# Kernel optimization log

Measured on AMD Instinct MI355X. Metric: run time of the kernel, lower is better.

## Reference

```python
import jax, jax.numpy as jnp
import numpy as np

P, N, D = 8, 1024, 768
H = 12
HS = D // H
SCALE = float(HS ** 0.5)  # NOTE: original multiplies by sqrt(head_size)


def setup_inputs() -> dict:
    key = jax.random.key(0)
    k1, k2, k3 = jax.random.split(key, 3)
    pixel_values = jax.random.normal(k1, (P, N, D), dtype=jnp.float32)
    attention_mask = jnp.zeros((P, 1, 1, N), dtype=jnp.float32)
    qkv_w = jax.random.normal(k2, (D, 3 * D), dtype=jnp.float32) * 0.02
    qkv_b = jnp.zeros((3 * D,), dtype=jnp.float32)
    proj_w = jax.random.normal(k3, (D, D), dtype=jnp.float32) * 0.02
    proj_b = jnp.zeros((D,), dtype=jnp.float32)
    return {
        "pixel_values": pixel_values,
        "attention_mask": attention_mask,
        "qkv_w": qkv_w,
        "qkv_b": qkv_b,
        "proj_w": proj_w,
        "proj_b": proj_b,
    }


def reference(pixel_values, attention_mask, qkv_w, qkv_b, proj_w, proj_b):
    p, n, d = pixel_values.shape
    # fused QKV projection: (p, n, 3d) -> (3, p, H, n, hs)
    mixed = pixel_values @ qkv_w + qkv_b
    mixed = mixed.reshape(p, n, 3, H, HS).transpose(2, 0, 3, 1, 4)
    q, k, v = mixed[0], mixed[1], mixed[2]
    # scores: (p, H, n, n); original multiplies by sqrt(head_size)
    scores = jnp.einsum("phqd,phkd->phqk", q, k) * SCALE
    probs = jax.nn.softmax(scores, axis=-1)
    # dropout p=0 (identity in eval); mask added POST-softmax, per source
    probs = probs + attention_mask
    ctx = jnp.einsum("phqk,phkd->phqd", probs, v)
    ctx = ctx.transpose(0, 2, 1, 3).reshape(p, n, d)
    out = ctx @ proj_w + proj_b
    return out
```

## Files before the change

### kernel.cpp

```cpp
#include <hip/hip_runtime.h>
#include <hip/hip_bf16.h>
#include <cstdint>
#include <math.h>

constexpr int PB = 8;
constexpr int NS = 1024;
constexpr int DM = 768;
constexpr int NH = 12;
constexpr int HSZ = 64;
constexpr float QS    = 11.541560327111707f;
constexpr float EOFFL = 126.95716359822878f;

typedef short    bf16x8 __attribute__((ext_vector_type(8)));
typedef _Float16 half8  __attribute__((ext_vector_type(8)));
typedef __fp16   fp16x2 __attribute__((ext_vector_type(2)));
typedef float    floatx4 __attribute__((ext_vector_type(4)));

#if __has_builtin(__builtin_amdgcn_exp2f)
#define EXP2(x) __builtin_amdgcn_exp2f(x)
#else
#define EXP2(x) exp2f(x)
#endif

__device__ __forceinline__ ushort f2h(float x) {
    _Float16 h = (_Float16)x;
    return *reinterpret_cast<ushort*>(&h);
}
__device__ __forceinline__ float h2f(ushort u) {
    _Float16 h = __builtin_bit_cast(_Float16, u);
    return (float)h;
}
__device__ __forceinline__ ushort f2bf(float x) {
    __hip_bfloat16 b = __float2bfloat16(x);
    return *reinterpret_cast<ushort*>(&b);
}
__device__ __forceinline__ float bf2f(ushort u) {
    __hip_bfloat16 b = *reinterpret_cast<__hip_bfloat16*>(&u);
    return __bfloat162float(b);
}
__device__ __forceinline__ unsigned int pk2h(float a, float b) {
    fp16x2 h = __builtin_amdgcn_cvt_pkrtz(a, b);
    return __builtin_bit_cast(unsigned int, h);
}

#define GLDS(g, l)                                                             \
    __builtin_amdgcn_global_load_lds(                                          \
        (const __attribute__((address_space(1))) void*)(g),                    \
        (__attribute__((address_space(3))) void*)(l), 16, 0, 0)

__global__ void split_kernel(const float* __restrict__ x, ushort* __restrict__ hf,
                             int n4)
{
    int i = blockIdx.x * blockDim.x + threadIdx.x;
    const int stride = gridDim.x * blockDim.x;
    for (; i < n4; i += stride) {
        const float4 v = ((const float4*)x)[i];
        ((ushort4*)hf)[i] = ushort4{f2h(v.x), f2h(v.y), f2h(v.z), f2h(v.w)};
    }
}

__global__ void splitT_kernel(const float* __restrict__ w, ushort* __restrict__ fT,
                              int K, int N)
{
    __shared__ float tile[32][33];
    const int tx = threadIdx.x, ty = threadIdx.y;
    const int bx = blockIdx.x, by = blockIdx.y;
    #pragma unroll
    for (int r = 0; r < 4; ++r)
        tile[ty + r*8][tx] = w[(size_t)(by*32 + ty + r*8) * N + bx*32 + tx];
    __syncthreads();
    #pragma unroll
    for (int r = 0; r < 4; ++r) {
        const int n = bx*32 + ty + r*8;
        const int k = by*32 + tx;
        fT[(size_t)n * K + k] = f2h(tile[tx][ty + r*8]);
    }
}

template <int MODE>
__global__ __launch_bounds__(256, 3)
void gemm_f16(const ushort* __restrict__ Af, const ushort* __restrict__ Bf,
              const float* __restrict__ bias, float* __restrict__ outf,
              ushort* __restrict__ qf, ushort* __restrict__ kf,
              ushort* __restrict__ vt, int K)
{
    __shared__ __align__(16) ushort As[128*64];
    __shared__ __align__(16) ushort Bs[128*64];

    const int t    = threadIdx.x;
    const int w    = t >> 6;
    const int lane = t & 63;
    const int l15  = lane & 15;
    const int quad = lane >> 4;
    const int wm = w >> 1, wn = w & 1;
    const int m0 = blockIdx.x * 128, n0 = blockIdx.y * 128;

    floatx4 acc[4][4];
    #pragma unroll
    for (int i = 0; i < 4; ++i)
        #pragma unroll
        for (int j = 0; j < 4; ++j) acc[i][j] = floatx4{0.f, 0.f, 0.f, 0.f};

    const int srow8 = lane >> 3;
    const int sslot = lane & 7;

    for (int k0 = 0; k0 < K; k0 += 64) {
        #pragma unroll
        for (int j = 0; j < 4; ++j) {
            const int row = w*32 + j*8 + srow8;
            const int seg = sslot ^ (row & 7);
            const int ldst = (w*32 + j*8) * 64;
            GLDS(Af + (size_t)(m0 + row) * K + k0 + seg*8, As + ldst);
            GLDS(Bf + (size_t)(n0 + row) * K + k0 + seg*8, Bs + ldst);
        }
        __syncthreads();

        #pragma unroll
        for (int h2 = 0; h2 < 2; ++h2) {
            half8 fa[4], fb[4];
            #pragma unroll
            for (int i = 0; i < 4; ++i) {
                const int sl = ((h2*4 + quad) ^ (l15 & 7)) * 8;
                fa[i] = *(const half8*)(As + (wm*64 + i*16 + l15) * 64 + sl);
                fb[i] = *(const half8*)(Bs + (wn*64 + i*16 + l15) * 64 + sl);
            }
            #pragma unroll
            for (int mt = 0; mt < 4; ++mt)
                #pragma unroll
                for (int nt = 0; nt < 4; ++nt)
                    acc[mt][nt] = __builtin_amdgcn_mfma_f32_16x16x32_f16(fa[mt], fb[nt], acc[mt][nt], 0, 0, 0);
        }
        __syncthreads();
    }

    if (MODE == 0) {
        #pragma unroll
        for (int nt = 0; nt < 4; ++nt) {
            const int col = n0 + wn*64 + nt*16 + l15;
            const float bval = bias[col];
            #pragma unroll
            for (int mt = 0; mt < 4; ++mt) {
                const int row0 = m0 + wm*64 + mt*16 + quad*4;
                #pragma unroll
                for (int r = 0; r < 4; ++r)
                    outf[(size_t)(row0 + r) * DM + col] = acc[mt][nt][r] + bval;
            }
        }
    } else {
        const int jbase = n0 + wn*64;
        const int c  = jbase / DM;
        const int hh = (jbase % DM) >> 6;
        const int pp = (m0 + wm*64) >> 10;
        const size_t head = (size_t)pp * NH + hh;
        if (c < 2) {
            ushort* dst = (c == 0 ? qf : kf);
            const float qscale = (c == 0) ? QS : 1.0f;
            #pragma unroll
            for (int nt = 0; nt < 4; ++nt) {
                const int s = nt*16 + l15;
                const float bval = bias[jbase + s];
                #pragma unroll
                for (int mt = 0; mt < 4; ++mt) {
                    const int tok0 = m0 + wm*64 + mt*16 + quad*4;
                    const int nn0  = tok0 & 1023;
                    #pragma unroll
                    for (int r = 0; r < 4; ++r)
                        dst[(head*NS + nn0 + r) * HSZ + s] = f2h((acc[mt][nt][r] + bval) * qscale);
                }
            }
        } else {
            #pragma unroll
            for (int nt = 0; nt < 4; ++nt) {
                const int s = nt*16 + l15;
                const float bval = bias[jbase + s];
                #pragma unroll
                for (int mt = 0; mt < 4; ++mt) {
                    const int tok0 = m0 + wm*64 + mt*16 + quad*4;
                    const int nn0  = tok0 & 1023;
                    ushort4 pk;
                    pk.x = f2bf(acc[mt][nt][0] + bval);
                    pk.y = f2bf(acc[mt][nt][1] + bval);
                    pk.z = f2bf(acc[mt][nt][2] + bval);
                    pk.w = f2bf(acc[mt][nt][3] + bval);
                    *(ushort4*)(vt + (head*HSZ + s) * NS + nn0) = pk;
                }
            }
        }
    }
}

__global__ void mv_kernel(const float* __restrict__ mask, const ushort* __restrict__ vt,
                          float* __restrict__ mv)
{
    __shared__ float red[4][64];
    const int ph = blockIdx.x;
    const int t  = threadIdx.x;
    const int c  = t & 63, part = t >> 6;
    const ushort* vrow = vt + ((size_t)ph * HSZ + c) * NS + part * 256;
    const float*  mrow = mask + (size_t)(ph / NH) * NS + part * 256;
    float acc = 0.f;
    for (int k = 0; k < 256; k += 4) {
        const ushort4 v4 = *(const ushort4*)(vrow + k);
        const float4  m4 = *(const float4*)(mrow + k);
        acc += m4.x * bf2f(v4.x) + m4.y * bf2f(v4.y)
             + m4.z * bf2f(v4.z) + m4.w * bf2f(v4.w);
    }
    red[part][c] = acc;
    __syncthreads();
    if (t < 64)
        mv[(size_t)ph * HSZ + t] = red[0][t] + red[1][t] + red[2][t] + red[3][t];
}

__global__ __launch_bounds__(256, 5)
void attn_mfma_kernel(const ushort* __restrict__ qf, const ushort* __restrict__ kf,
                      const ushort* __restrict__ vt, const float* __restrict__ mv,
                      ushort* __restrict__ ctx)
{
    __shared__ __align__(16) ushort khs[64*64];
    __shared__ __align__(16) ushort vs [64*64];

    const int t    = threadIdx.x;
    const int w    = t >> 6;
    const int lane = t & 63;
    const int l15  = lane & 15;
    const int quad = lane >> 4;
    const int ph = blockIdx.x, qt = blockIdx.y;
    const int h  = ph % NH,    p  = ph / NH;
    const size_t headoff = ((size_t)p * NH + h) * (size_t)(NS * HSZ);

    const ushort* qb = qf + headoff + (size_t)(qt*64 + w*16 + l15) * HSZ + quad*8;
    const half8 qfr0 = *(const half8*)(qb);
    const half8 qfr1 = *(const half8*)(qb + 32);

    floatx4 o[4];
    float lsum = 0.f;
    #pragma unroll
    for (int tc = 0; tc < 4; ++tc) o[tc] = floatx4{0.f, 0.f, 0.f, 0.f};

    const int srow8 = lane >> 3;
    const int sslot = lane & 7;
    const int xs = l15 & 7;

    for (int kt = 0; kt < 16; ++kt) {
        __syncthreads();
        #pragma unroll
        for (int j = 0; j < 2; ++j) {
            const int row  = w*16 + j*8 + srow8;
            const int segK = sslot ^ ((row & 3) | (((row >> 3) & 1) << 2));
            const int segV = sslot ^ (row & 7);
            const size_t gk = headoff + (size_t)(kt*64 + row) * HSZ + segK*8;
            const size_t gv = headoff + (size_t)row * NS + kt*64 + segV*8;
            const int ldst = (w*16 + j*8) * 64;
            GLDS(kf + gk, khs + ldst);
            GLDS(vt + gv, vs  + ldst);
        }
        __syncthreads();

        bf16x8 bp[2];
        #pragma unroll
        for (int tt = 0; tt < 4; ++tt) {
            const int rho = ((l15 >> 2) << 3) + ((tt & 1) << 2) + (l15 & 3) + ((tt >> 1) << 5);
            const int a0 = rho*64 + ((quad       ^ xs) * 8);
            const int a1 = rho*64 + (((quad | 4) ^ xs) * 8);
            const half8 bh0 = *(const half8*)(khs + a0);
            const half8 bh1 = *(const half8*)(khs + a1);
            floatx4 a = floatx4{-EOFFL, -EOFFL, -EOFFL, -EOFFL};
            a = __builtin_amdgcn_mfma_f32_16x16x32_f16(bh0, qfr0, a, 0, 0, 0);
            a = __builtin_amdgcn_mfma_f32_16x16x32_f16(bh1, qfr1, a, 0, 0, 0);
            const float e0 = EXP2(a[0]);
            const float e1 = EXP2(a[1]);
            const float e2 = EXP2(a[2]);
            const float e3 = EXP2(a[3]);
            lsum += (e0 + e1) + (e2 + e3);
            bf16x8& dst = bp[tt >> 1];
            const int off = (tt & 1) * 4;
            dst[off + 0] = (short)f2bf(e0);
            dst[off + 1] = (short)f2bf(e1);
            dst[off + 2] = (short)f2bf(e2);
            dst[off + 3] = (short)f2bf(e3);
        }

        #pragma unroll
        for (int tc = 0; tc < 4; ++tc) {
            const int crow = (tc*16 + l15) * 64;
            const bf16x8 va0 = *(const bf16x8*)(vs + crow + ((quad       ^ xs) * 8));
            const bf16x8 va1 = *(const bf16x8*)(vs + crow + (((quad | 4) ^ xs) * 8));
            o[tc] = __builtin_amdgcn_mfma_f32_16x16x32_bf16(va0, bp[0], o[tc], 0, 0, 0);
            o[tc] = __builtin_amdgcn_mfma_f32_16x16x32_bf16(va1, bp[1], o[tc], 0, 0, 0);
        }
    }

    float l = lsum;
    l += __shfl_xor(l, 16);
    l += __shfl_xor(l, 32);
    const float inv = 1.0f / l;

    const float* mvp = mv + ((size_t)p * NH + h) * HSZ;
    const int row = qt*64 + w*16 + l15;
    const size_t base = ((size_t)p * NS + row) * DM + h * 64;
    #pragma unroll
    for (int tc = 0; tc < 4; ++tc) {
        const int c0 = tc*16 + quad*4;
        const unsigned int lo = pk2h(o[tc][0] * inv + mvp[c0 + 0],
                                     o[tc][1] * inv + mvp[c0 + 1]);
        const unsigned int hi = pk2h(o[tc][2] * inv + mvp[c0 + 2],
                                     o[tc][3] * inv + mvp[c0 + 3]);
        uint2 st; st.x = lo; st.y = hi;
        *(uint2*)(ctx + base + c0) = st;
    }
}

extern "C" void kernel_launch(void* const* d_in, const int* in_sizes, int n_in,
                              void* d_out, int out_size, void* d_ws, size_t ws_size,
                              hipStream_t stream)
{
    const float* x      = (const float*)d_in[0];
    const float* mask   = (const float*)d_in[1];
    const float* qkv_w  = (const float*)d_in[2];
    const float* qkv_b  = (const float*)d_in[3];
    const float* proj_w = (const float*)d_in[4];
    const float* proj_b = (const float*)d_in[5];
    float* out = (float*)d_out;

    const size_t HE = (size_t)PB * NH * NS * HSZ;
    const size_t QW = (size_t)DM * 3 * DM;
    const size_t PW = (size_t)DM * DM;
    ushort* xf  = (ushort*)d_ws;
    ushort* qwf = xf + HE;
    ushort* pwf = qwf + QW;
    ushort* qfv = pwf + PW;
    ushort* kfv = qfv + HE;
    ushort* vtv = kfv + HE;
    float*  mvb = (float*)(vtv + HE);
    ushort* cth = xf;

    split_kernel<<<2048, 256, 0, stream>>>(x, xf, (int)(HE / 4));
    splitT_kernel<<<dim3(3*DM/32, DM/32), dim3(32, 8), 0, stream>>>(qkv_w, qwf, DM, 3*DM);
    splitT_kernel<<<dim3(DM/32,   DM/32), dim3(32, 8), 0, stream>>>(proj_w, pwf, DM, DM);

    gemm_f16<1><<<dim3(PB*NS/128, 3*DM/128), 256, 0, stream>>>(
        xf, qwf, qkv_b, nullptr, qfv, kfv, vtv, DM);

    mv_kernel<<<dim3(PB*NH), 256, 0, stream>>>(mask, vtv, mvb);

    attn_mfma_kernel<<<dim3(PB*NH, NS/64), 256, 0, stream>>>(
        qfv, kfv, vtv, mvb, cth);

    gemm_f16<0><<<dim3(PB*NS/128, DM/128), 256, 0, stream>>>(
        cth, pwf, proj_b, out, nullptr, nullptr, nullptr, DM);
}
```

Measured before the change: 201.0 us.

## Process two query tiles per attention block to reuse staged K/V tiles

```diff
diff --git a/kernel.cpp b/kernel.cpp
--- a/kernel.cpp
+++ b/kernel.cpp
@@ -78,7 +78,7 @@
 }
 
 template <int MODE>
-__global__ __launch_bounds__(256, 3)
+__global__ __launch_bounds__(256, 5)
 void gemm_f16(const ushort* __restrict__ Af, const ushort* __restrict__ Bf,
               const float* __restrict__ bias, float* __restrict__ outf,
               ushort* __restrict__ qf, ushort* __restrict__ kf,
@@ -211,7 +211,7 @@
         mv[(size_t)ph * HSZ + t] = red[0][t] + red[1][t] + red[2][t] + red[3][t];
 }
 
-__global__ __launch_bounds__(256, 5)
+__global__ __launch_bounds__(256, 3)
 void attn_mfma_kernel(const ushort* __restrict__ qf, const ushort* __restrict__ kf,
                       const ushort* __restrict__ vt, const float* __restrict__ mv,
                       ushort* __restrict__ ctx)
@@ -228,14 +228,20 @@
     const int h  = ph % NH,    p  = ph / NH;
     const size_t headoff = ((size_t)p * NH + h) * (size_t)(NS * HSZ);
 
-    const ushort* qb = qf + headoff + (size_t)(qt*64 + w*16 + l15) * HSZ + quad*8;
-    const half8 qfr0 = *(const half8*)(qb);
-    const half8 qfr1 = *(const half8*)(qb + 32);
-
-    floatx4 o[4];
-    float lsum = 0.f;
-    #pragma unroll
-    for (int tc = 0; tc < 4; ++tc) o[tc] = floatx4{0.f, 0.f, 0.f, 0.f};
+    const ushort* qpa = qf + headoff + (size_t)(qt*128 + w*16 + l15) * HSZ + quad*8;
+    const half8 qa0 = *(const half8*)(qpa);
+    const half8 qa1 = *(const half8*)(qpa + 32);
+    const ushort* qpb = qpa + (size_t)64 * HSZ;
+    const half8 qb0 = *(const half8*)(qpb);
+    const half8 qb1 = *(const half8*)(qpb + 32);
+
+    floatx4 oA[4], oB[4];
+    float lsumA = 0.f, lsumB = 0.f;
+    #pragma unroll
+    for (int tc = 0; tc < 4; ++tc) {
+        oA[tc] = floatx4{0.f, 0.f, 0.f, 0.f};
+        oB[tc] = floatx4{0.f, 0.f, 0.f, 0.f};
+    }
 
     const int srow8 = lane >> 3;
     const int sslot = lane & 7;
@@ -256,7 +262,7 @@
         }
         __syncthreads();
 
-        bf16x8 bp[2];
+        bf16x8 bpA[2], bpB[2];
         #pragma unroll
         for (int tt = 0; tt < 4; ++tt) {
             const int rho = ((l15 >> 2) << 3) + ((tt & 1) << 2) + (l15 & 3) + ((tt >> 1) << 5);
@@ -264,20 +270,33 @@
             const int a1 = rho*64 + (((quad | 4) ^ xs) * 8);
             const half8 bh0 = *(const half8*)(khs + a0);
             const half8 bh1 = *(const half8*)(khs + a1);
-            floatx4 a = floatx4{-EOFFL, -EOFFL, -EOFFL, -EOFFL};
-            a = __builtin_amdgcn_mfma_f32_16x16x32_f16(bh0, qfr0, a, 0, 0, 0);
-            a = __builtin_amdgcn_mfma_f32_16x16x32_f16(bh1, qfr1, a, 0, 0, 0);
-            const float e0 = EXP2(a[0]);
-            const float e1 = EXP2(a[1]);
-            const float e2 = EXP2(a[2]);
-            const float e3 = EXP2(a[3]);
-            lsum += (e0 + e1) + (e2 + e3);
-            bf16x8& dst = bp[tt >> 1];
+            floatx4 sA = floatx4{-EOFFL, -EOFFL, -EOFFL, -EOFFL};
+            sA = __builtin_amdgcn_mfma_f32_16x16x32_f16(bh0, qa0, sA, 0, 0, 0);
+            sA = __builtin_amdgcn_mfma_f32_16x16x32_f16(bh1, qa1, sA, 0, 0, 0);
+            floatx4 sB = floatx4{-EOFFL, -EOFFL, -EOFFL, -EOFFL};
+            sB = __builtin_amdgcn_mfma_f32_16x16x32_f16(bh0, qb0, sB, 0, 0, 0);
+            sB = __builtin_amdgcn_mfma_f32_16x16x32_f16(bh1, qb1, sB, 0, 0, 0);
+            const float a0e = EXP2(sA[0]);
+            const float a1e = EXP2(sA[1]);
+            const float a2e = EXP2(sA[2]);
+            const float a3e = EXP2(sA[3]);
+            lsumA += (a0e + a1e) + (a2e + a3e);
+            const float b0e = EXP2(sB[0]);
+            const float b1e = EXP2(sB[1]);
+            const float b2e = EXP2(sB[2]);
+            const float b3e = EXP2(sB[3]);
+            lsumB += (b0e + b1e) + (b2e + b3e);
             const int off = (tt & 1) * 4;
-            dst[off + 0] = (short)f2bf(e0);
-            dst[off + 1] = (short)f2bf(e1);
-            dst[off + 2] = (short)f2bf(e2);
-            dst[off + 3] = (short)f2bf(e3);
+            bf16x8& dA = bpA[tt >> 1];
+            dA[off + 0] = (short)f2bf(a0e);
+            dA[off + 1] = (short)f2bf(a1e);
+            dA[off + 2] = (short)f2bf(a2e);
+            dA[off + 3] = (short)f2bf(a3e);
+            bf16x8& dB = bpB[tt >> 1];
+            dB[off + 0] = (short)f2bf(b0e);
+            dB[off + 1] = (short)f2bf(b1e);
+            dB[off + 2] = (short)f2bf(b2e);
+            dB[off + 3] = (short)f2bf(b3e);
         }
 
         #pragma unroll
@@ -285,28 +304,39 @@
             const int crow = (tc*16 + l15) * 64;
             const bf16x8 va0 = *(const bf16x8*)(vs + crow + ((quad       ^ xs) * 8));
             const bf16x8 va1 = *(const bf16x8*)(vs + crow + (((quad | 4) ^ xs) * 8));
-            o[tc] = __builtin_amdgcn_mfma_f32_16x16x32_bf16(va0, bp[0], o[tc], 0, 0, 0);
-            o[tc] = __builtin_amdgcn_mfma_f32_16x16x32_bf16(va1, bp[1], o[tc], 0, 0, 0);
-        }
-    }
-
-    float l = lsum;
-    l += __shfl_xor(l, 16);
-    l += __shfl_xor(l, 32);
-    const float inv = 1.0f / l;
+            oA[tc] = __builtin_amdgcn_mfma_f32_16x16x32_bf16(va0, bpA[0], oA[tc], 0, 0, 0);
+            oA[tc] = __builtin_amdgcn_mfma_f32_16x16x32_bf16(va1, bpA[1], oA[tc], 0, 0, 0);
+            oB[tc] = __builtin_amdgcn_mfma_f32_16x16x32_bf16(va0, bpB[0], oB[tc], 0, 0, 0);
+            oB[tc] = __builtin_amdgcn_mfma_f32_16x16x32_bf16(va1, bpB[1], oB[tc], 0, 0, 0);
+        }
+    }
+
+    float lA = lsumA;
+    lA += __shfl_xor(lA, 16);
+    lA += __shfl_xor(lA, 32);
+    const float invA = 1.0f / lA;
+    float lB = lsumB;
+    lB += __shfl_xor(lB, 16);
+    lB += __shfl_xor(lB, 32);
+    const float invB = 1.0f / lB;
 
     const float* mvp = mv + ((size_t)p * NH + h) * HSZ;
-    const int row = qt*64 + w*16 + l15;
-    const size_t base = ((size_t)p * NS + row) * DM + h * 64;
+    const int rowA = qt*128 + w*16 + l15;
+    const size_t baseA = ((size_t)p * NS + rowA) * DM + h * 64;
+    const size_t baseB = baseA + (size_t)64 * DM;
     #pragma unroll
     for (int tc = 0; tc < 4; ++tc) {
         const int c0 = tc*16 + quad*4;
-        const unsigned int lo = pk2h(o[tc][0] * inv + mvp[c0 + 0],
-                                     o[tc][1] * inv + mvp[c0 + 1]);
-        const unsigned int hi = pk2h(o[tc][2] * inv + mvp[c0 + 2],
-                                     o[tc][3] * inv + mvp[c0 + 3]);
-        uint2 st; st.x = lo; st.y = hi;
-        *(uint2*)(ctx + base + c0) = st;
+        const float m0v = mvp[c0 + 0], m1v = mvp[c0 + 1];
+        const float m2v = mvp[c0 + 2], m3v = mvp[c0 + 3];
+        uint2 stA;
+        stA.x = pk2h(oA[tc][0] * invA + m0v, oA[tc][1] * invA + m1v);
+        stA.y = pk2h(oA[tc][2] * invA + m2v, oA[tc][3] * invA + m3v);
+        *(uint2*)(ctx + baseA + c0) = stA;
+        uint2 stB;
+        stB.x = pk2h(oB[tc][0] * invB + m0v, oB[tc][1] * invB + m1v);
+        stB.y = pk2h(oB[tc][2] * invB + m2v, oB[tc][3] * invB + m3v);
+        *(uint2*)(ctx + baseB + c0) = stB;
     }
 }
 
@@ -343,7 +373,7 @@
 
     mv_kernel<<<dim3(PB*NH), 256, 0, stream>>>(mask, vtv, mvb);
 
-    attn_mfma_kernel<<<dim3(PB*NH, NS/64), 256, 0, stream>>>(
+    attn_mfma_kernel<<<dim3(PB*NH, NS/128), 256, 0, stream>>>(
         qfv, kfv, vtv, mvb, cth);
 
     gemm_f16<0><<<dim3(PB*NS/128, DM/128), 256, 0, stream>>>(
```

New measurement: 281.6 us. 1.4x slower.
